# Performance work log

Hardware: AMD Instinct MI355X
Metric: run time of the kernel (lower is better)

The kernel has to match this reference:

```python
import jax, jax.numpy as jnp
import numpy as np

NUM_BINS = 8
TAIL = 3.0
MIN_BW = 1e-3   # min_bin_width
MIN_BH = 1e-3   # min_bin_height
MIN_D = 1e-3    # min_derivative
EPS = 1e-6      # searchsorted eps
N = 4_194_304


def setup_inputs() -> dict:
    key = jax.random.key(0)
    k1, k2 = jax.random.split(key)
    inputs = jax.random.normal(k1, (N,), dtype=jnp.float32)
    params = jax.random.normal(k2, (N, 3 * NUM_BINS + 1), dtype=jnp.float32)
    return {"inputs": inputs, "params": params}


def _cum_knots(unnorm, min_size):
    # softmax * 2B, then affine rescale (faithful to the torch source, even
    # though it is a nonstandard normalization), cumsum, pad with -B, pin last to B.
    B, K = TAIL, NUM_BINS
    w = jax.nn.softmax(unnorm, axis=-1) * (2.0 * B)
    w = w * (2.0 * B - K * min_size) + min_size
    c = jnp.cumsum(w, axis=-1)
    c = jnp.concatenate([jnp.full(c.shape[:-1] + (1,), -B, c.dtype), c], axis=-1)
    return c.at[..., -1].set(B)


def _gather(a, idx):
    return jnp.take_along_axis(a, idx[:, None], axis=-1)[:, 0]


def reference(inputs, params):
    K, B = NUM_BINS, TAIL
    x = inputs.reshape(-1)
    uw = params[..., :K]
    uh = params[..., K:2 * K]
    ud = params[..., 2 * K:]              # [N, K+1]

    inside = (x >= -B) & (x <= B)
    # clamp for the spline branch so masked-out lanes stay finite (identical
    # math for inside elements)
    xi = jnp.clip(x, -B, B)

    cumwidths = _cum_knots(uw, MIN_BW)     # [N, K+1]
    cumheights = _cum_knots(uh, MIN_BH)    # [N, K+1]
    derivs = jax.nn.softplus(ud) + MIN_D   # [N, K+1]

    # searchsorted: last knot nudged by eps, count of (x >= knot) - 1
    bin_loc = cumwidths.at[..., -1].add(EPS)
    idx = jnp.sum((xi[:, None] >= bin_loc).astype(jnp.int32), axis=-1) - 1
    idx = jnp.clip(idx, 0, K - 1)

    cw_k = _gather(cumwidths, idx)
    cw_k1 = _gather(cumwidths, idx + 1)
    ch_k = _gather(cumheights, idx)
    ch_k1 = _gather(cumheights, idx + 1)
    d_k = _gather(derivs, idx)
    d_k1 = _gather(derivs, idx + 1)

    bw = cw_k1 - cw_k
    bh = ch_k1 - ch_k
    theta = (xi - cw_k) / bw
    t1m = theta * (1.0 - theta)
    numerator = bh * (d_k * theta ** 2 + d_k1 * t1m)
    denominator = d_k * theta ** 2 + 2.0 * d_k1 * t1m + (1.0 - theta) ** 2
    out_inside = ch_k + numerator / denominator
    deriv_numerator = d_k1 * d_k * bh * denominator ** 2
    ld_inside = jnp.log(deriv_numerator / (bw * denominator ** 2))

    # outside the interval: identity with log|det| = log(first derivative)
    ld_outside = jnp.log(derivs[..., 0])

    outputs = jnp.where(inside, out_inside, x)
    log_abs_det = jnp.where(inside, ld_inside, ld_outside)
    return outputs.reshape(inputs.shape), log_abs_det.sum()
```

## Files before the change

### kernel.cpp

```cpp
#include <hip/hip_runtime.h>
#include <math.h>


#define TAILB 3.0f
#define MINSZ 0.001f
#define NBLOCKS 768
#define NTILES 16384
#define TILE_F4 1600
#define BUF_F4 1664
#define BUF_F 6656

typedef unsigned int u32;

__device__ __forceinline__ void gload_lds16(const void* g, void* l) {
    __builtin_amdgcn_global_load_lds(
        (const __attribute__((address_space(1))) u32*)g,
        (__attribute__((address_space(3))) u32*)l,
        16, 0, 0);
}

__device__ __forceinline__ float frcp(float x) {
    return __builtin_amdgcn_rcpf(x);
}

__device__ __forceinline__ float softplus_d(float u) {
    return fmaxf(u, 0.0f) + __logf(1.0f + __expf(-fabsf(u))) + MINSZ;
}

__device__ __forceinline__ void stage_tile(const float4* __restrict__ params4,
                                           const float4* __restrict__ x4,
                                           float4* ldsbuf, int tile, int tid)
{
    const float4* psrc = params4 + (size_t)tile * TILE_F4;
    #pragma unroll
    for (int v = 0; v < 6; ++v) {
        const int q = tid + v * 256;
        gload_lds16(psrc + q, ldsbuf + q);
    }
    const int q = 1536 + tid;
    if (q < 1600) {
        gload_lds16(psrc + q, ldsbuf + q);
    } else if (q < 1664) {
        gload_lds16(x4 + (size_t)tile * 64 + (q - 1600), ldsbuf + q);
    } else {
        gload_lds16(psrc + tid, ldsbuf + tid);
    }
}

__launch_bounds__(256, 3)
__global__ void rqs_kernel(const float* __restrict__ x_in,
                           const float* __restrict__ params,
                           float* __restrict__ out,
                           float* __restrict__ partial)
{
    __shared__ __align__(16) float lds[2 * BUF_F];
    __shared__ float wsum[4];

    const int tid = threadIdx.x;
    const int bid = blockIdx.x;
    const float4* params4 = (const float4*)params;
    const float4* x4 = (const float4*)x_in;
    const float fac_num = (2.0f * TAILB) * (2.0f * TAILB - 8.0f * MINSZ);

    float accv = 0.0f;

    stage_tile(params4, x4, (float4*)lds, bid, tid);

    int k = 0;
    for (int t = bid; t < NTILES; t += NBLOCKS, ++k) {
        const int cur = k & 1;
        const int tn = (t + NBLOCKS < NTILES) ? (t + NBLOCKS) : t;
        stage_tile(params4, x4, (float4*)&lds[(cur ^ 1) * BUF_F], tn, tid);

        asm volatile("s_waitcnt vmcnt(7)" ::: "memory");
        __builtin_amdgcn_s_barrier();

        const float* row = &lds[cur * BUF_F + tid * 25];
        const float x = lds[cur * BUF_F + 6400 + tid];
        const float xi = fminf(fmaxf(x, -TAILB), TAILB);

        float ew[8];
        float s = 0.0f;
        #pragma unroll
        for (int j = 0; j < 8; ++j) { ew[j] = __expf(row[j]); s += ew[j]; }
        const float facw = fac_num * frcp(s);

        float c = 0.0f;
        int idx = 0;
        float cw_k = -TAILB, cw_k1 = TAILB;
        bool found = false;
        #pragma unroll
        for (int j = 0; j < 7; ++j) {
            c = fmaf(ew[j], facw, c + MINSZ);
            const bool ge = (xi >= c);
            idx += ge ? 1 : 0;
            cw_k  = ge ? c : cw_k;
            cw_k1 = (!ge && !found) ? c : cw_k1;
            found = found || !ge;
        }

        float ch_k = -TAILB, ch_k1 = TAILB;
        {
            float eh[8];
            float sh = 0.0f;
            #pragma unroll
            for (int j = 0; j < 8; ++j) { eh[j] = __expf(row[8 + j]); sh += eh[j]; }
            const float fach = fac_num * frcp(sh);
            c = 0.0f;
            #pragma unroll
            for (int j = 1; j <= 7; ++j) {
                c = fmaf(eh[j - 1], fach, c + MINSZ);
                ch_k  = (idx == j)     ? c : ch_k;
                ch_k1 = (idx + 1 == j) ? c : ch_k1;
            }
        }

        const float d_k  = softplus_d(row[16 + idx]);
        const float d_k1 = softplus_d(row[17 + idx]);

        const float bw  = cw_k1 - cw_k;
        const float bh  = ch_k1 - ch_k;
        const float rbw = frcp(bw);
        const float th  = (xi - cw_k) * rbw;
        const float omt = 1.0f - th;
        const float th2 = th * th;
        const float t1m = th * omt;
        const float num = bh * fmaf(d_k, th2, d_k1 * t1m);
        const float den = fmaf(2.0f * d_k1, t1m, fmaf(d_k, th2, omt * omt));
        const float out_in = fmaf(num, frcp(den), ch_k);

        const bool inside = (x >= -TAILB) && (x <= TAILB);
        __builtin_nontemporal_store(inside ? out_in : x, &out[t * 256 + tid]);

        float ldarg = d_k1 * d_k * bh * rbw;
        if (!__all(inside)) {
            const float d0 = softplus_d(row[16]);
            ldarg = inside ? ldarg : d0;
        }
        accv += __logf(ldarg);

        __builtin_amdgcn_s_barrier();
    }

    float acc = accv;
    #pragma unroll
    for (int off = 32; off > 0; off >>= 1)
        acc += __shfl_down(acc, off);
    const int wave = tid >> 6, lane = tid & 63;
    if (lane == 0) wsum[wave] = acc;
    __syncthreads();
    if (tid == 0)
        partial[bid] = (wsum[0] + wsum[1]) + (wsum[2] + wsum[3]);
}

__global__ void rqs_reduce(const float* __restrict__ partial, int nb,
                           float* __restrict__ out_sum)
{
    const int tid = threadIdx.x;
    double acc = 0.0;
    for (int q = tid; q < nb; q += 256)
        acc += (double)partial[q];
    #pragma unroll
    for (int off = 32; off > 0; off >>= 1)
        acc += __shfl_down(acc, off);
    __shared__ double wsum[4];
    const int wave = tid >> 6, lane = tid & 63;
    if (lane == 0) wsum[wave] = acc;
    __syncthreads();
    if (tid == 0)
        *out_sum = (float)((wsum[0] + wsum[1]) + (wsum[2] + wsum[3]));
}

extern "C" void kernel_launch(void* const* d_in, const int* in_sizes, int n_in,
                              void* d_out, int out_size, void* d_ws, size_t ws_size,
                              hipStream_t stream) {
    const float* x      = (const float*)d_in[0];
    const float* params = (const float*)d_in[1];
    float* out = (float*)d_out;
    const int n = in_sizes[0];
    float* partial = (float*)d_ws;

    hipLaunchKernelGGL(rqs_kernel, dim3(NBLOCKS), dim3(256), 0, stream,
                       x, params, out, partial);
    hipLaunchKernelGGL(rqs_reduce, dim3(1), dim3(256), 0, stream,
                       partial, NBLOCKS, out + n);
}
```

Measured before the change: 89.15 us.

## Give each wave its own double-buffered LDS pipeline and drop block barriers

Restructures staging so each wavefront loads and processes its own 64-row tiles through a private double buffer, replacing the block-wide barriers with per-wave vmcnt waits. Tiles are assigned to waves as contiguous ranges with a fat/thin split instead of grid striding. This is meant to remove barrier stalls where waves wait on each other and to let memory loads overlap more freely. The risk is smaller per-request batches and more dependence on correct vmcnt accounting, including the outstanding stores.

Result: slower. 100.2 us (+12.4%).

```diff
diff --git a/kernel.cpp b/kernel.cpp
--- a/kernel.cpp
+++ b/kernel.cpp
@@ -4,11 +4,10 @@
 
 #define TAILB 3.0f
 #define MINSZ 0.001f
-#define NBLOCKS 768
-#define NTILES 16384
-#define TILE_F4 1600
-#define BUF_F4 1664
-#define BUF_F 6656
+#define NBLK 768
+#define NWAVES 3072
+#define NTILES 65536
+#define NFAT 1024
 
 typedef unsigned int u32;
 
@@ -27,23 +26,18 @@
     return fmaxf(u, 0.0f) + __logf(1.0f + __expf(-fabsf(u))) + MINSZ;
 }
 
-__device__ __forceinline__ void stage_tile(const float4* __restrict__ params4,
-                                           const float4* __restrict__ x4,
-                                           float4* ldsbuf, int tile, int tid)
+__device__ __forceinline__ void stage(const float4* __restrict__ p4g,
+                                      const float4* __restrict__ x4g,
+                                      float* buf, int tile, int lane)
 {
-    const float4* psrc = params4 + (size_t)tile * TILE_F4;
+    const float4* ps = p4g + (size_t)tile * 400;
+    float4* bd = (float4*)buf;
     #pragma unroll
-    for (int v = 0; v < 6; ++v) {
-        const int q = tid + v * 256;
-        gload_lds16(psrc + q, ldsbuf + q);
-    }
-    const int q = 1536 + tid;
-    if (q < 1600) {
-        gload_lds16(psrc + q, ldsbuf + q);
-    } else if (q < 1664) {
-        gload_lds16(x4 + (size_t)tile * 64 + (q - 1600), ldsbuf + q);
-    } else {
-        gload_lds16(psrc + tid, ldsbuf + tid);
+    for (int v = 0; v < 6; ++v)
+        gload_lds16(ps + v * 64 + lane, bd + v * 64 + lane);
+    if (lane < 16) {
+        gload_lds16(ps + 384 + lane, bd + 384 + lane);
+        gload_lds16(x4g + (size_t)tile * 16 + lane, bd + 400 + lane);
     }
 }
 
@@ -53,30 +47,41 @@
                            float* __restrict__ out,
                            float* __restrict__ partial)
 {
-    __shared__ __align__(16) float lds[2 * BUF_F];
+    __shared__ __align__(16) float lds[4][2][1664];
     __shared__ float wsum[4];
 
-    const int tid = threadIdx.x;
-    const int bid = blockIdx.x;
-    const float4* params4 = (const float4*)params;
-    const float4* x4 = (const float4*)x_in;
+    const int tid  = threadIdx.x;
+    const int wid  = tid >> 6;
+    const int lane = tid & 63;
+    const int gw   = blockIdx.x * 4 + wid;
+
+    const int nt = (gw < NFAT) ? 22 : 21;
+    const int t0 = (gw < NFAT) ? gw * 22 : NFAT * 22 + (gw - NFAT) * 21;
+
+    const float4* p4g = (const float4*)params;
+    const float4* x4g = (const float4*)x_in;
+    float* bufA = &lds[wid][0][0];
+    float* bufB = &lds[wid][1][0];
+
     const float fac_num = (2.0f * TAILB) * (2.0f * TAILB - 8.0f * MINSZ);
-
     float accv = 0.0f;
 
-    stage_tile(params4, x4, (float4*)lds, bid, tid);
+    stage(p4g, x4g, bufA, t0, lane);
 
-    int k = 0;
-    for (int t = bid; t < NTILES; t += NBLOCKS, ++k) {
-        const int cur = k & 1;
-        const int tn = (t + NBLOCKS < NTILES) ? (t + NBLOCKS) : t;
-        stage_tile(params4, x4, (float4*)&lds[(cur ^ 1) * BUF_F], tn, tid);
+    for (int k = 0; k < nt; ++k) {
+        const int t = t0 + k;
+        float* cur = (k & 1) ? bufB : bufA;
+        float* nxt = (k & 1) ? bufA : bufB;
 
-        asm volatile("s_waitcnt vmcnt(7)" ::: "memory");
-        __builtin_amdgcn_s_barrier();
+        if (k + 1 < nt) {
+            stage(p4g, x4g, nxt, t + 1, lane);
+            asm volatile("s_waitcnt vmcnt(8)" ::: "memory");
+        } else {
+            asm volatile("s_waitcnt vmcnt(1)" ::: "memory");
+        }
 
-        const float* row = &lds[cur * BUF_F + tid * 25];
-        const float x = lds[cur * BUF_F + 6400 + tid];
+        const float* row = cur + lane * 25;
+        const float x = cur[1600 + lane];
         const float xi = fminf(fmaxf(x, -TAILB), TAILB);
 
         float ew[8];
@@ -130,7 +135,8 @@
         const float out_in = fmaf(num, frcp(den), ch_k);
 
         const bool inside = (x >= -TAILB) && (x <= TAILB);
-        __builtin_nontemporal_store(inside ? out_in : x, &out[t * 256 + tid]);
+        __builtin_nontemporal_store(inside ? out_in : x,
+                                    &out[(size_t)t * 64 + lane]);
 
         float ldarg = d_k1 * d_k * bh * rbw;
         if (!__all(inside)) {
@@ -138,19 +144,16 @@
             ldarg = inside ? ldarg : d0;
         }
         accv += __logf(ldarg);
-
-        __builtin_amdgcn_s_barrier();
     }
 
     float acc = accv;
     #pragma unroll
     for (int off = 32; off > 0; off >>= 1)
         acc += __shfl_down(acc, off);
-    const int wave = tid >> 6, lane = tid & 63;
-    if (lane == 0) wsum[wave] = acc;
+    if (lane == 0) wsum[wid] = acc;
     __syncthreads();
     if (tid == 0)
-        partial[bid] = (wsum[0] + wsum[1]) + (wsum[2] + wsum[3]);
+        partial[blockIdx.x] = (wsum[0] + wsum[1]) + (wsum[2] + wsum[3]);
 }
 
 __global__ void rqs_reduce(const float* __restrict__ partial, int nb,
@@ -163,12 +166,12 @@
     #pragma unroll
     for (int off = 32; off > 0; off >>= 1)
         acc += __shfl_down(acc, off);
-    __shared__ double wsum[4];
+    __shared__ double dsum[4];
     const int wave = tid >> 6, lane = tid & 63;
-    if (lane == 0) wsum[wave] = acc;
+    if (lane == 0) dsum[wave] = acc;
     __syncthreads();
     if (tid == 0)
-        *out_sum = (float)((wsum[0] + wsum[1]) + (wsum[2] + wsum[3]));
+        *out_sum = (float)((dsum[0] + dsum[1]) + (dsum[2] + dsum[3]));
 }
 
 extern "C" void kernel_launch(void* const* d_in, const int* in_sizes, int n_in,
@@ -180,8 +183,8 @@
     const int n = in_sizes[0];
     float* partial = (float*)d_ws;
 
-    hipLaunchKernelGGL(rqs_kernel, dim3(NBLOCKS), dim3(256), 0, stream,
+    hipLaunchKernelGGL(rqs_kernel, dim3(NBLK), dim3(256), 0, stream,
                        x, params, out, partial);
     hipLaunchKernelGGL(rqs_reduce, dim3(1), dim3(256), 0, stream,
-                       partial, NBLOCKS, out + n);
+                       partial, NBLK, out + n);
 }
```
